# Kernel optimization log

Hardware: AMD Instinct MI355X
Metric: run time of the kernel (lower is better)

Reference implementation:

```python
import jax, jax.numpy as jnp
import numpy as np

LR = 0.1  # inner-loop learning rate from `param - 0.1 * grad`

D = 4096          # memory width d; key/val are (1, d) per docstring
CTX = 512         # loss_context_size: number of keys per update step


def setup_inputs() -> dict:
    key = jax.random.key(0)
    k1, k2, k3 = jax.random.split(key, 3)
    W = jax.random.normal(k1, (D, D), dtype=jnp.float32) / np.sqrt(D)
    keys = jax.random.normal(k2, (CTX, D), dtype=jnp.float32)
    vals = jax.random.normal(k3, (CTX, D), dtype=jnp.float32)
    return {"W": W, "keys": keys, "vals": vals}


def reference(W, keys, vals):
    # OneStep.forward: preds_i = functional_forward(key_i, (W,)) = key_i @ W,
    # loss = MSE(preds, vals); new_W = W - 0.1 * dloss/dW.
    # The per-key loop is batched into a single (CTX, D) x (D, D) matmul.
    def loss_fn(Wp):
        preds = keys @ Wp  # (CTX, D)
        return jnp.mean((preds - vals) ** 2)

    g = jax.grad(loss_fn)(W)
    return W - LR * g
```

## Files before the change

kernel.cpp:

```cpp
#include <hip/hip_runtime.h>
#include <hip/hip_bf16.h>


typedef __bf16 bf16_t;
typedef __bf16 bf16x8 __attribute__((ext_vector_type(8)));
typedef float f32x4 __attribute__((ext_vector_type(4)));

#define D_DIM 4096
#define CTX_N 512
#define UPD_SCALE 9.5367431640625e-8f

__device__ __forceinline__ void gld16(const bf16_t* g, bf16_t* l) {
    __builtin_amdgcn_global_load_lds(
        (const __attribute__((address_space(1))) void*)g,
        (__attribute__((address_space(3))) void*)l, 16, 0, 0);
}

__device__ __forceinline__ void t_body(
    float* tile, const float* __restrict__ src, bf16_t* __restrict__ dstT,
    bf16_t* __restrict__ dstN, int N, int bx, int by)
{
    const int tid = threadIdx.x;
    const int C0 = bx * 64, R0 = by * 64;
    const int r  = tid >> 2, cs = (tid & 3) * 16;

    const float* s = src + (size_t)(R0 + r) * N + C0 + cs;
    float f[16];
#pragma unroll
    for (int u = 0; u < 4; ++u) {
        const float4 v = ((const float4*)s)[u];
        f[4 * u + 0] = v.x; f[4 * u + 1] = v.y; f[4 * u + 2] = v.z; f[4 * u + 3] = v.w;
    }
#pragma unroll
    for (int u = 0; u < 16; ++u) tile[r * 65 + cs + u] = f[u];

    if (dstN) {
        bf16x8 v0, v1;
#pragma unroll
        for (int u = 0; u < 8; ++u) { v0[u] = (bf16_t)f[u]; v1[u] = (bf16_t)f[8 + u]; }
        bf16_t* d = dstN + (size_t)(R0 + r) * N + C0 + cs;
        *(bf16x8*)d = v0; *(bf16x8*)(d + 8) = v1;
    }
    __syncthreads();

    bf16x8 o0, o1;
#pragma unroll
    for (int u = 0; u < 8; ++u) {
        o0[u] = (bf16_t)tile[(cs + u) * 65 + r];
        o1[u] = (bf16_t)tile[(cs + 8 + u) * 65 + r];
    }
    bf16_t* d = dstT + (size_t)(C0 + r) * (dstN || N == D_DIM ? 0 : 0);
    (void)d;
    {
    }
    ;
}

__device__ __forceinline__ void t_body2(
    float* tile, const float* __restrict__ src, bf16_t* __restrict__ dstT,
    bf16_t* __restrict__ dstN, int M, int N, int bx, int by)
{
    const int tid = threadIdx.x;
    const int C0 = bx * 64, R0 = by * 64;
    const int r  = tid >> 2, cs = (tid & 3) * 16;

    const float* s = src + (size_t)(R0 + r) * N + C0 + cs;
    float f[16];
#pragma unroll
    for (int u = 0; u < 4; ++u) {
        const float4 v = ((const float4*)s)[u];
        f[4 * u + 0] = v.x; f[4 * u + 1] = v.y; f[4 * u + 2] = v.z; f[4 * u + 3] = v.w;
    }
#pragma unroll
    for (int u = 0; u < 16; ++u) tile[r * 65 + cs + u] = f[u];

    if (dstN) {
        bf16x8 v0, v1;
#pragma unroll
        for (int u = 0; u < 8; ++u) { v0[u] = (bf16_t)f[u]; v1[u] = (bf16_t)f[8 + u]; }
        bf16_t* d = dstN + (size_t)(R0 + r) * N + C0 + cs;
        *(bf16x8*)d = v0; *(bf16x8*)(d + 8) = v1;
    }
    __syncthreads();

    bf16x8 o0, o1;
#pragma unroll
    for (int u = 0; u < 8; ++u) {
        o0[u] = (bf16_t)tile[(cs + u) * 65 + r];
        o1[u] = (bf16_t)tile[(cs + 8 + u) * 65 + r];
    }
    bf16_t* d = dstT + (size_t)(C0 + r) * M + R0 + cs;
    *(bf16x8*)d = o0; *(bf16x8*)(d + 8) = o1;
}

__global__ __launch_bounds__(256) void t_all(
    const float* __restrict__ W, const float* __restrict__ K,
    const float* __restrict__ V, bf16_t* __restrict__ Wt,
    bf16_t* __restrict__ Kt, bf16_t* __restrict__ Kb, bf16_t* __restrict__ Vt)
{
    __shared__ float tile[64 * 65];
    const int y = blockIdx.y;
    if (y < 64)      t_body2(tile, W, Wt, nullptr, D_DIM, D_DIM, blockIdx.x, y);
    else if (y < 72) t_body2(tile, K, Kt, Kb,      CTX_N, D_DIM, blockIdx.x, y - 64);
    else             t_body2(tile, V, Vt, nullptr, CTX_N, D_DIM, blockIdx.x, y - 72);
}


__global__ __launch_bounds__(256) void k1_residual(
    const bf16_t* __restrict__ Wt, const bf16_t* __restrict__ Kb,
    const bf16_t* __restrict__ Vt, bf16_t* __restrict__ Rt)
{
    __shared__ __align__(16) char smem[32768];

    const int tid = threadIdx.x, wave = tid >> 6, lane = tid & 63;
    const int j0 = blockIdx.x * 64, c0 = blockIdx.y * 64;
    const int l15 = lane & 15, quad = lane >> 4;
    const int kw = wave * 1024;

    bf16_t* As = (bf16_t*)(smem + wave * 4096);
    bf16_t* Bs = (bf16_t*)(smem + 16384 + wave * 4096);

    f32x4 acc[4][4] = {};

    const int srow = lane >> 2, sseg = (lane & 3) * 8;
    const bf16_t* ga = Wt + (size_t)(j0 + srow) * D_DIM + kw + sseg;
    const bf16_t* gb = Kb + (size_t)(c0 + srow) * D_DIM + kw + sseg;
    bf16_t* la = As + lane * 8;
    bf16_t* lb = Bs + lane * 8;

    for (int i = 0; i < 32; ++i) {
        const int ko = i * 32;
#pragma unroll
        for (int c = 0; c < 4; ++c)
            gld16(ga + ko + (size_t)(c * 16) * D_DIM, la + c * 512);
#pragma unroll
        for (int c = 0; c < 4; ++c)
            gld16(gb + ko + (size_t)(c * 16) * D_DIM, lb + c * 512);
        __builtin_amdgcn_s_waitcnt(0x0f74);
        bf16x8 a[4];
#pragma unroll
        for (int mi = 0; mi < 4; ++mi)
            a[mi] = *(const bf16x8*)(As + (mi * 16 + l15) * 32 + quad * 8);
        __builtin_amdgcn_s_waitcnt(0x0f70);
        bf16x8 b[4];
#pragma unroll
        for (int ni = 0; ni < 4; ++ni)
            b[ni] = *(const bf16x8*)(Bs + (ni * 16 + l15) * 32 + quad * 8);
#pragma unroll
        for (int mi = 0; mi < 4; ++mi)
#pragma unroll
            for (int ni = 0; ni < 4; ++ni)
                acc[mi][ni] = __builtin_amdgcn_mfma_f32_16x16x32_bf16(
                    a[mi], b[ni], acc[mi][ni], 0, 0, 0);
    }

    float* ep = (float*)smem;
    __syncthreads();
#pragma unroll
    for (int w = 0; w < 4; ++w) {
        if (wave == w) {
#pragma unroll
            for (int mi = 0; mi < 4; ++mi)
#pragma unroll
                for (int ni = 0; ni < 4; ++ni)
#pragma unroll
                    for (int r = 0; r < 4; ++r) {
                        const int row = mi * 16 + quad * 4 + r;
                        const int col = ni * 16 + l15;
                        if (w == 0) ep[row * 68 + col]  = acc[mi][ni][r];
                        else        ep[row * 68 + col] += acc[mi][ni][r];
                    }
        }
        __syncthreads();
    }

    {
        const int row = tid >> 2, cs = (tid & 3) * 16;
        const size_t rbase = (size_t)(j0 + row) * CTX_N + c0 + cs;
        float e[16];
#pragma unroll
        for (int u = 0; u < 4; ++u) {
            const float4 v = ((const float4*)(ep + row * 68 + cs))[u];
            e[4 * u + 0] = v.x; e[4 * u + 1] = v.y;
            e[4 * u + 2] = v.z; e[4 * u + 3] = v.w;
        }
        const bf16x8 v0 = *(const bf16x8*)(Vt + rbase);
        const bf16x8 v1 = *(const bf16x8*)(Vt + rbase + 8);
        bf16x8 o0, o1;
#pragma unroll
        for (int u = 0; u < 8; ++u) {
            o0[u] = (bf16_t)(e[u]     - (float)v0[u]);
            o1[u] = (bf16_t)(e[8 + u] - (float)v1[u]);
        }
        *(bf16x8*)(Rt + rbase)     = o0;
        *(bf16x8*)(Rt + rbase + 8) = o1;
    }
}

__global__ __launch_bounds__(256) void k2_update(
    const bf16_t* __restrict__ Kt, const bf16_t* __restrict__ Rt,
    const float* __restrict__ W, float* __restrict__ out)
{
    __shared__ __align__(16) char smem[32 * 132 * 4];

    bf16_t* As = (bf16_t*)smem;
    bf16_t* Bs = (bf16_t*)(smem + 8192);
    float*  ep = (float*)smem;

    const int tid = threadIdx.x;
    const int j0 = blockIdx.x * 128, i0 = blockIdx.y * 128;
    const int lane = tid & 63, wave = tid >> 6;
    const int wi = (wave >> 1) * 64, wj = (wave & 1) * 64;
    const int l15 = lane & 15, quad = lane >> 4;

    f32x4 acc[4][4] = {};

    const bf16_t* ga = Kt + (size_t)(i0 + (tid >> 2)) * CTX_N + (tid & 3) * 8;
    const bf16_t* gb = Rt + (size_t)(j0 + (tid >> 2)) * CTX_N + (tid & 3) * 8;
    bf16_t* la = (bf16_t*)(smem + tid * 16);
    bf16_t* lb = (bf16_t*)(smem + 8192 + tid * 16);

    for (int cc = 0; cc < CTX_N; cc += 32) {
        gld16(ga + cc, la);
        gld16(ga + cc + (size_t)64 * CTX_N, la + 64 * 32);
        gld16(gb + cc, lb);
        gld16(gb + cc + (size_t)64 * CTX_N, lb + 64 * 32);
        __syncthreads();
        bf16x8 a[4], b[4];
#pragma unroll
        for (int mi = 0; mi < 4; ++mi)
            a[mi] = *(const bf16x8*)(As + (wi + mi * 16 + l15) * 32 + quad * 8);
#pragma unroll
        for (int ni = 0; ni < 4; ++ni)
            b[ni] = *(const bf16x8*)(Bs + (wj + ni * 16 + l15) * 32 + quad * 8);
#pragma unroll
        for (int mi = 0; mi < 4; ++mi)
#pragma unroll
            for (int ni = 0; ni < 4; ++ni)
                acc[mi][ni] = __builtin_amdgcn_mfma_f32_16x16x32_bf16(
                    a[mi], b[ni], acc[mi][ni], 0, 0, 0);
        __syncthreads();
    }

    const int row = tid >> 3;
    const int cb  = (tid & 7) * 16;
#pragma unroll
    for (int p = 0; p < 4; ++p) {
        const float* wrow = W + (size_t)(i0 + p * 32 + row) * D_DIM + j0 + cb;
        float4 wv[4];
#pragma unroll
        for (int u = 0; u < 4; ++u) wv[u] = ((const float4*)wrow)[u];

        if ((wave >> 1) == (p >> 1)) {
#pragma unroll
            for (int mh = 0; mh < 2; ++mh) {
                const int mi = (p & 1) * 2 + mh;
#pragma unroll
                for (int ni = 0; ni < 4; ++ni)
#pragma unroll
                    for (int r = 0; r < 4; ++r)
                        ep[(mh * 16 + quad * 4 + r) * 132 + wj + ni * 16 + l15] =
                            acc[mi][ni][r];
            }
        }
        __syncthreads();
        {
            float* orow = out + (size_t)(i0 + p * 32 + row) * D_DIM + j0 + cb;
            const float* erow = ep + row * 132 + cb;
#pragma unroll
            for (int u = 0; u < 4; ++u) {
                const float4 ev = ((const float4*)erow)[u];
                float4 ov;
                ov.x = wv[u].x - UPD_SCALE * ev.x;
                ov.y = wv[u].y - UPD_SCALE * ev.y;
                ov.z = wv[u].z - UPD_SCALE * ev.z;
                ov.w = wv[u].w - UPD_SCALE * ev.w;
                ((float4*)orow)[u] = ov;
            }
        }
        __syncthreads();
    }
}

extern "C" void kernel_launch(void* const* d_in, const int* in_sizes, int n_in,
                              void* d_out, int out_size, void* d_ws, size_t ws_size,
                              hipStream_t stream) {
    const float* W = (const float*)d_in[0];
    const float* K = (const float*)d_in[1];
    const float* V = (const float*)d_in[2];
    float* out = (float*)d_out;

    char* ws = (char*)d_ws;
    bf16_t* Wt = (bf16_t*)(ws);
    bf16_t* Kt = (bf16_t*)(ws + (size_t)32 * 1024 * 1024);
    bf16_t* Kb = (bf16_t*)(ws + (size_t)36 * 1024 * 1024);
    bf16_t* Vt = (bf16_t*)(ws + (size_t)40 * 1024 * 1024);
    bf16_t* Rt = (bf16_t*)(ws + (size_t)44 * 1024 * 1024);

    t_all      <<<dim3(64, 80), 256, 0, stream>>>(W, K, V, Wt, Kt, Kb, Vt);
    k1_residual<<<dim3(64, 8),  256, 0, stream>>>(Wt, Kb, Vt, Rt);
    k2_update  <<<dim3(32, 32), 256, 0, stream>>>(Kt, Rt, W, out);
}
```

Before: 210.4 us.

## Double-buffer LDS tiles in both GEMM kernels to overlap loads with MFMA

```diff
diff --git a/kernel.cpp b/kernel.cpp
--- a/kernel.cpp
+++ b/kernel.cpp
@@ -14,46 +14,6 @@
     __builtin_amdgcn_global_load_lds(
         (const __attribute__((address_space(1))) void*)g,
         (__attribute__((address_space(3))) void*)l, 16, 0, 0);
-}
-
-__device__ __forceinline__ void t_body(
-    float* tile, const float* __restrict__ src, bf16_t* __restrict__ dstT,
-    bf16_t* __restrict__ dstN, int N, int bx, int by)
-{
-    const int tid = threadIdx.x;
-    const int C0 = bx * 64, R0 = by * 64;
-    const int r  = tid >> 2, cs = (tid & 3) * 16;
-
-    const float* s = src + (size_t)(R0 + r) * N + C0 + cs;
-    float f[16];
-#pragma unroll
-    for (int u = 0; u < 4; ++u) {
-        const float4 v = ((const float4*)s)[u];
-        f[4 * u + 0] = v.x; f[4 * u + 1] = v.y; f[4 * u + 2] = v.z; f[4 * u + 3] = v.w;
-    }
-#pragma unroll
-    for (int u = 0; u < 16; ++u) tile[r * 65 + cs + u] = f[u];
-
-    if (dstN) {
-        bf16x8 v0, v1;
-#pragma unroll
-        for (int u = 0; u < 8; ++u) { v0[u] = (bf16_t)f[u]; v1[u] = (bf16_t)f[8 + u]; }
-        bf16_t* d = dstN + (size_t)(R0 + r) * N + C0 + cs;
-        *(bf16x8*)d = v0; *(bf16x8*)(d + 8) = v1;
-    }
-    __syncthreads();
-
-    bf16x8 o0, o1;
-#pragma unroll
-    for (int u = 0; u < 8; ++u) {
-        o0[u] = (bf16_t)tile[(cs + u) * 65 + r];
-        o1[u] = (bf16_t)tile[(cs + 8 + u) * 65 + r];
-    }
-    bf16_t* d = dstT + (size_t)(C0 + r) * (dstN || N == D_DIM ? 0 : 0);
-    (void)d;
-    {
-    }
-    ;
 }
 
 __device__ __forceinline__ void t_body2(
@@ -106,53 +66,75 @@
 }
 
 
+
+#define K1_COMPUTE(BSEL, WA, WB)                                             \
+    {                                                                        \
+        const bf16_t* As = (const bf16_t*)(reg + (BSEL) * 8192);             \
+        const bf16_t* Bs = (const bf16_t*)(reg + 4096 + (BSEL) * 8192);      \
+        __builtin_amdgcn_s_waitcnt(WA);                                      \
+        bf16x8 af[4];                                                        \
+        _Pragma("unroll")                                                    \
+        for (int mi = 0; mi < 4; ++mi)                                       \
+            af[mi] = *(const bf16x8*)(As + (mi * 16 + l15) * 32 + quad * 8); \
+        __builtin_amdgcn_s_waitcnt(WB);                                      \
+        bf16x8 bq[4];                                                        \
+        _Pragma("unroll")                                                    \
+        for (int ni = 0; ni < 4; ++ni)                                       \
+            bq[ni] = *(const bf16x8*)(Bs + (ni * 16 + l15) * 32 + quad * 8); \
+        _Pragma("unroll")                                                    \
+        for (int mi = 0; mi < 4; ++mi)                                       \
+            _Pragma("unroll")                                                \
+            for (int ni = 0; ni < 4; ++ni)                                   \
+                acc[mi][ni] = __builtin_amdgcn_mfma_f32_16x16x32_bf16(       \
+                    af[mi], bq[ni], acc[mi][ni], 0, 0, 0);                   \
+    }
+
 __global__ __launch_bounds__(256) void k1_residual(
     const bf16_t* __restrict__ Wt, const bf16_t* __restrict__ Kb,
     const bf16_t* __restrict__ Vt, bf16_t* __restrict__ Rt)
 {
-    __shared__ __align__(16) char smem[32768];
+    __shared__ __align__(16) char smem[65536];
 
     const int tid = threadIdx.x, wave = tid >> 6, lane = tid & 63;
     const int j0 = blockIdx.x * 64, c0 = blockIdx.y * 64;
     const int l15 = lane & 15, quad = lane >> 4;
     const int kw = wave * 1024;
 
-    bf16_t* As = (bf16_t*)(smem + wave * 4096);
-    bf16_t* Bs = (bf16_t*)(smem + 16384 + wave * 4096);
+    char* reg = smem + wave * 16384;
 
     f32x4 acc[4][4] = {};
 
     const int srow = lane >> 2, sseg = (lane & 3) * 8;
     const bf16_t* ga = Wt + (size_t)(j0 + srow) * D_DIM + kw + sseg;
     const bf16_t* gb = Kb + (size_t)(c0 + srow) * D_DIM + kw + sseg;
-    bf16_t* la = As + lane * 8;
-    bf16_t* lb = Bs + lane * 8;
-
-    for (int i = 0; i < 32; ++i) {
-        const int ko = i * 32;
+
+    auto stageA = [&](int bsel, int ko) {
+        bf16_t* la = (bf16_t*)(reg + bsel * 8192) + lane * 8;
 #pragma unroll
         for (int c = 0; c < 4; ++c)
             gld16(ga + ko + (size_t)(c * 16) * D_DIM, la + c * 512);
+    };
+    auto stageB = [&](int bsel, int ko) {
+        bf16_t* lb = (bf16_t*)(reg + 4096 + bsel * 8192) + lane * 8;
 #pragma unroll
         for (int c = 0; c < 4; ++c)
             gld16(gb + ko + (size_t)(c * 16) * D_DIM, lb + c * 512);
-        __builtin_amdgcn_s_waitcnt(0x0f74);
-        bf16x8 a[4];
-#pragma unroll
-        for (int mi = 0; mi < 4; ++mi)
-            a[mi] = *(const bf16x8*)(As + (mi * 16 + l15) * 32 + quad * 8);
-        __builtin_amdgcn_s_waitcnt(0x0f70);
-        bf16x8 b[4];
-#pragma unroll
-        for (int ni = 0; ni < 4; ++ni)
-            b[ni] = *(const bf16x8*)(Bs + (ni * 16 + l15) * 32 + quad * 8);
-#pragma unroll
-        for (int mi = 0; mi < 4; ++mi)
-#pragma unroll
-            for (int ni = 0; ni < 4; ++ni)
-                acc[mi][ni] = __builtin_amdgcn_mfma_f32_16x16x32_bf16(
-                    a[mi], b[ni], acc[mi][ni], 0, 0, 0);
-    }
+    };
+
+    stageA(0, 0); stageB(0, 0);
+#pragma unroll 1
+    for (int t = 1; t <= 29; t += 2) {
+        stageA(1, t * 32); stageB(1, t * 32);
+        __builtin_amdgcn_sched_barrier(0);
+        K1_COMPUTE(0, 0x0f7c, 0x0f78);
+        stageA(0, (t + 1) * 32); stageB(0, (t + 1) * 32);
+        __builtin_amdgcn_sched_barrier(0);
+        K1_COMPUTE(1, 0x0f7c, 0x0f78);
+    }
+    stageA(1, 31 * 32); stageB(1, 31 * 32);
+    __builtin_amdgcn_sched_barrier(0);
+    K1_COMPUTE(0, 0x0f7c, 0x0f78);
+    K1_COMPUTE(1, 0x0f74, 0x0f70);
 
     float* ep = (float*)smem;
     __syncthreads();
@@ -197,15 +179,31 @@
     }
 }
 
+
+#define K2_COMPUTE(BSEL)                                                     \
+    {                                                                        \
+        const bf16_t* As = (const bf16_t*)(smem + (BSEL) * 16384);           \
+        const bf16_t* Bs = (const bf16_t*)(smem + (BSEL) * 16384 + 8192);    \
+        bf16x8 af[4], bq[4];                                                 \
+        _Pragma("unroll")                                                    \
+        for (int mi = 0; mi < 4; ++mi)                                       \
+            af[mi] = *(const bf16x8*)(As + (wi + mi * 16 + l15) * 32 + quad * 8); \
+        _Pragma("unroll")                                                    \
+        for (int ni = 0; ni < 4; ++ni)                                       \
+            bq[ni] = *(const bf16x8*)(Bs + (wj + ni * 16 + l15) * 32 + quad * 8); \
+        _Pragma("unroll")                                                    \
+        for (int mi = 0; mi < 4; ++mi)                                       \
+            _Pragma("unroll")                                                \
+            for (int ni = 0; ni < 4; ++ni)                                   \
+                acc[mi][ni] = __builtin_amdgcn_mfma_f32_16x16x32_bf16(       \
+                    af[mi], bq[ni], acc[mi][ni], 0, 0, 0);                   \
+    }
+
 __global__ __launch_bounds__(256) void k2_update(
     const bf16_t* __restrict__ Kt, const bf16_t* __restrict__ Rt,
     const float* __restrict__ W, float* __restrict__ out)
 {
-    __shared__ __align__(16) char smem[32 * 132 * 4];
-
-    bf16_t* As = (bf16_t*)smem;
-    bf16_t* Bs = (bf16_t*)(smem + 8192);
-    float*  ep = (float*)smem;
+    __shared__ __align__(16) char smem[32768];
 
     const int tid = threadIdx.x;
     const int j0 = blockIdx.x * 128, i0 = blockIdx.y * 128;
@@ -217,31 +215,37 @@
 
     const bf16_t* ga = Kt + (size_t)(i0 + (tid >> 2)) * CTX_N + (tid & 3) * 8;
     const bf16_t* gb = Rt + (size_t)(j0 + (tid >> 2)) * CTX_N + (tid & 3) * 8;
-    bf16_t* la = (bf16_t*)(smem + tid * 16);
-    bf16_t* lb = (bf16_t*)(smem + 8192 + tid * 16);
-
-    for (int cc = 0; cc < CTX_N; cc += 32) {
+
+    auto stage = [&](int bsel, int cc) {
+        bf16_t* la = (bf16_t*)(smem + bsel * 16384) + tid * 8;
+        bf16_t* lb = (bf16_t*)(smem + bsel * 16384 + 8192) + tid * 8;
         gld16(ga + cc, la);
         gld16(ga + cc + (size_t)64 * CTX_N, la + 64 * 32);
         gld16(gb + cc, lb);
         gld16(gb + cc + (size_t)64 * CTX_N, lb + 64 * 32);
-        __syncthreads();
-        bf16x8 a[4], b[4];
-#pragma unroll
-        for (int mi = 0; mi < 4; ++mi)
-            a[mi] = *(const bf16x8*)(As + (wi + mi * 16 + l15) * 32 + quad * 8);
-#pragma unroll
-        for (int ni = 0; ni < 4; ++ni)
-            b[ni] = *(const bf16x8*)(Bs + (wj + ni * 16 + l15) * 32 + quad * 8);
-#pragma unroll
-        for (int mi = 0; mi < 4; ++mi)
-#pragma unroll
-            for (int ni = 0; ni < 4; ++ni)
-                acc[mi][ni] = __builtin_amdgcn_mfma_f32_16x16x32_bf16(
-                    a[mi], b[ni], acc[mi][ni], 0, 0, 0);
-        __syncthreads();
-    }
-
+    };
+
+    stage(0, 0);
+    __syncthreads();
+#pragma unroll 1
+    for (int t = 1; t <= 13; t += 2) {
+        stage(1, t * 32);
+        __builtin_amdgcn_sched_barrier(0);
+        K2_COMPUTE(0);
+        __syncthreads();
+        stage(0, (t + 1) * 32);
+        __builtin_amdgcn_sched_barrier(0);
+        K2_COMPUTE(1);
+        __syncthreads();
+    }
+    stage(1, 15 * 32);
+    __builtin_amdgcn_sched_barrier(0);
+    K2_COMPUTE(0);
+    __syncthreads();
+    K2_COMPUTE(1);
+    __syncthreads();
+
+    float* ep = (float*)smem;
     const int row = tid >> 3;
     const int cb  = (tid & 7) * 16;
 #pragma unroll
```

Measured after the change: 206.5 us. Within noise of the previous version (-1.8%).
